# Kernel optimization log

Hardware: AMD Instinct MI355X
Metric: run time of the kernel (lower is better)

## Reference

```python
import jax, jax.numpy as jnp
import numpy as np

B, S, D = 2, 2048, 1024
H, Dh = 16, 64  # qkv_features=1024, head_dim=64
F = 1024        # out_features


def setup_inputs() -> dict:
    key = jax.random.key(0)
    ks = jax.random.split(key, 16)
    s = 0.02
    return {
        'inputs_q': jax.random.normal(ks[0], (B, S, D), jnp.float32),
        'inputs_kv': jax.random.normal(ks[1], (B, S, D), jnp.float32),
        'pos_embed': jax.random.normal(ks[2], (S, D), jnp.float32),
        'Wq': jax.random.normal(ks[3], (D, H, Dh), jnp.float32) * s,
        'bq': jnp.zeros((H, Dh), jnp.float32),
        'Wk': jax.random.normal(ks[4], (D, H, Dh), jnp.float32) * s,
        'bk': jnp.zeros((H, Dh), jnp.float32),
        'Wv': jax.random.normal(ks[5], (D, H, Dh), jnp.float32) * s,
        'bv': jnp.zeros((H, Dh), jnp.float32),
        'Wpos': jax.random.normal(ks[6], (D, H, Dh), jnp.float32) * s,
        'r_r_bias': jax.random.normal(ks[7], (H, Dh), jnp.float32) * s,
        'r_w_bias': jax.random.normal(ks[8], (H, Dh), jnp.float32) * s,
        'Wout': jax.random.normal(ks[9], (H, Dh, F), jnp.float32) * s,
        'bout': jnp.zeros((F,), jnp.float32),
    }


_roll_vmap = jax.vmap(jnp.roll, in_axes=(-2, 0, None), out_axes=-2)


def reference(inputs_q, inputs_kv, pos_embed, Wq, bq, Wk, bk, Wv, bv,
              Wpos, r_r_bias, r_w_bias, Wout, bout):
    # QKV projections: [B,S,D] x [D,H,Dh] -> [B,S,H,Dh]
    q = jnp.einsum('bsd,dhk->bshk', inputs_q, Wq) + bq
    k = jnp.einsum('bsd,dhk->bshk', inputs_kv, Wk) + bk
    v = jnp.einsum('bsd,dhk->bshk', inputs_kv, Wv) + bv
    # relative position embedding projection: [S,D] -> [S,H,Dh]
    r_pos = jnp.einsum('sd,dhk->shk', pos_embed, Wpos)

    q_len = q.shape[-3]
    depth = q.shape[-1]
    # content score + relative-position score, both [B,H,S,S]
    aw = jnp.einsum('bqhd,bkhd->bhqk', q + r_w_bias, k)
    aw_r = jnp.einsum('bqhd,khd->bhqk', q + r_r_bias, r_pos)
    # Transformer-XL relative shift: per query-row roll along key axis
    shifts = jnp.arange(0, q_len) - (q_len - 1)
    aw_r = _roll_vmap(aw_r, shifts, -1)
    aw = (aw + aw_r) / jnp.sqrt(depth).astype(aw.dtype)
    attn = jax.nn.softmax(aw, axis=-1)
    # weighted sum: [B,S,H,Dh]
    x = jnp.einsum('bhqk,bkhd->bqhd', attn, v)
    # output projection contracting (H,Dh)
    out = jnp.einsum('bqhd,hdf->bqf', x, Wout) + bout
    return out
```

## Files before the change

kernel.cpp:

```cpp
#include <hip/hip_runtime.h>
#include <hip/hip_bf16.h>
#include <hip/hip_fp16.h>


#define B_  2
#define S_  2048
#define D_  1024
#define H_  16
#define DH_ 64
#define HD_ 1024
#define F_  1024
#define N_  4096
#define KC_ 512
#define SP2 516
#define KQSC 0.1803368801111204f

typedef __attribute__((ext_vector_type(8))) short  short8;
typedef __attribute__((ext_vector_type(4))) float  floatx4;
typedef __attribute__((ext_vector_type(4))) unsigned int uintx4;

__device__ __forceinline__ unsigned short f2bf(float x) {
  unsigned u = __float_as_uint(x);
  u += 0x7FFFu + ((u >> 16) & 1u);
  return (unsigned short)(u >> 16);
}
__device__ __forceinline__ unsigned short f2h(float x) {
  __half h = __float2half(x);
  unsigned short u; __builtin_memcpy(&u, &h, 2);
  return u;
}
__device__ __forceinline__ float h2f(unsigned short u) {
  __half h; __builtin_memcpy(&h, &u, 2);
  return __half2float(h);
}

#define CQ_ (N_ * D_ / 4)
#define CAST_BLKS 10240
struct PrepP {
  const float* sq; const float* skv; const float* spos;
  unsigned short* dq; unsigned short* dkv; unsigned short* dpos;
  const float* ts[5]; unsigned short* td[5];
};
__global__ void prep_all(PrepP p) {
  __shared__ float t[32][33];
  int bid = blockIdx.x;
  int tid = threadIdx.x;
  if (bid < CAST_BLKS) {
    int i = bid * 256 + tid;
    const float* s; unsigned short* d; int off;
    if (i < CQ_)            { s = p.sq;   d = p.dq;   off = i; }
    else if (i < 2 * CQ_)   { s = p.skv;  d = p.dkv;  off = i - CQ_; }
    else                    { s = p.spos; d = p.dpos; off = i - 2 * CQ_; }
    float4 v = ((const float4*)s)[off];
    ((ushort4*)d)[off] = make_ushort4(f2bf(v.x), f2bf(v.y), f2bf(v.z), f2bf(v.w));
  } else {
    int b2 = bid - CAST_BLKS;
    int z = b2 >> 10, y = (b2 >> 5) & 31, x = b2 & 31;
    const float* src = p.ts[z];
    unsigned short* dst = p.td[z];
    int c0 = x * 32, r0 = y * 32;
    int tx = tid & 31, ty = tid >> 5;
#pragma unroll
    for (int i = 0; i < 4; i++)
      t[ty + i * 8][tx] = src[(size_t)(r0 + ty + i * 8) * 1024 + c0 + tx];
    __syncthreads();
#pragma unroll
    for (int i = 0; i < 4; i++)
      dst[(size_t)(c0 + ty + i * 8) * 1024 + r0 + tx] = f2bf(t[tx][ty + i * 8]);
  }
}

struct GSeg {
  const unsigned short* A; const unsigned short* Bt;
  const float* bias; const float* b2a; const float* b2b;
  unsigned short* outA; unsigned short* outB; float* outF;
  int mode; int bend;
};
struct GP { GSeg s[4]; };
__launch_bounds__(256, 2)
__global__ void gemm_bt(GP p, int Nn, int K) {
  __shared__ unsigned short As[128 * 64];
  __shared__ unsigned short Bs[128 * 64];
  int bx = blockIdx.x;
  GSeg g = p.s[0]; int base = 0;
  if (bx >= p.s[0].bend) { g = p.s[1]; base = p.s[0].bend; }
  if (bx >= p.s[1].bend) { g = p.s[2]; base = p.s[1].bend; }
  if (bx >= p.s[2].bend) { g = p.s[3]; base = p.s[2].bend; }
  bx -= base;
  int nb = Nn >> 7;
  int bm = bx / nb, bn = bx % nb;
  int tid = threadIdx.x;
  int lane = tid & 63, wv = tid >> 6;
  int wm = wv >> 1, wn = wv & 1;
  int lm = lane & 15, lg = lane >> 4;
  const unsigned short* Ab = g.A + (size_t)(bm * 128) * K;
  const unsigned short* Bb = g.Bt + (size_t)(bn * 128) * K;
  floatx4 acc[4][4];
#pragma unroll
  for (int i = 0; i < 4; i++)
#pragma unroll
    for (int j = 0; j < 4; j++) acc[i][j] = (floatx4){0.f, 0.f, 0.f, 0.f};

  int lr = tid >> 3;
  int lc = (tid & 7) * 8;
  for (int k0 = 0; k0 < K; k0 += 64) {
    __syncthreads();
#pragma unroll
    for (int i = 0; i < 4; i++) {
      int r = i * 32 + lr;
      *(uint4*)&As[r * 64 + lc] = *(const uint4*)&Ab[(size_t)r * K + k0 + lc];
      *(uint4*)&Bs[r * 64 + lc] = *(const uint4*)&Bb[(size_t)r * K + k0 + lc];
    }
    __syncthreads();
#pragma unroll
    for (int kk = 0; kk < 2; kk++) {
      short8 af[4], bf[4];
#pragma unroll
      for (int i = 0; i < 4; i++)
        af[i] = *(const short8*)&As[(wm * 64 + i * 16 + lm) * 64 + kk * 32 + lg * 8];
#pragma unroll
      for (int j = 0; j < 4; j++)
        bf[j] = *(const short8*)&Bs[(wn * 64 + j * 16 + lm) * 64 + kk * 32 + lg * 8];
#pragma unroll
      for (int i = 0; i < 4; i++)
#pragma unroll
        for (int j = 0; j < 4; j++)
          acc[i][j] = __builtin_amdgcn_mfma_f32_16x16x32_bf16(af[i], bf[j], acc[i][j], 0, 0, 0);
    }
  }
#pragma unroll
  for (int j = 0; j < 4; j++) {
    int col = bn * 128 + wn * 64 + j * 16 + lm;
    float bs = g.bias ? g.bias[col] : 0.f;
    float ba = g.b2a ? g.b2a[col] : 0.f;
    float bb = g.b2b ? g.b2b[col] : 0.f;
#pragma unroll
    for (int i = 0; i < 4; i++) {
      int row0 = bm * 128 + wm * 64 + i * 16 + lg * 4;
      if (g.mode == 4) {
        int s = row0 & 2047, bb2 = row0 >> 11;
        size_t vidx = (((size_t)bb2 * H_ + (col >> 6)) * 64 + (col & 63)) * (size_t)S_ + s;
        ushort4 o = make_ushort4(f2bf(acc[i][j][0] + bs), f2bf(acc[i][j][1] + bs),
                                 f2bf(acc[i][j][2] + bs), f2bf(acc[i][j][3] + bs));
        *(ushort4*)&g.outA[vidx] = o;
      } else {
#pragma unroll
        for (int r = 0; r < 4; r++) {
          float v = acc[i][j][r] + bs;
          size_t idx = (size_t)(row0 + r) * Nn + col;
          if (g.mode == 0)      g.outA[idx] = f2bf(v);
          else if (g.mode == 1) { g.outA[idx] = f2bf((v + ba) * KQSC); g.outB[idx] = f2bf((v + bb) * KQSC); }
          else                  g.outF[idx] = v;
        }
      }
    }
  }
}

__launch_bounds__(512, 4)
__global__ void attn_kernel(const unsigned short* __restrict__ qw,
                            const unsigned short* __restrict__ qr,
                            const unsigned short* __restrict__ kb,
                            const unsigned short* __restrict__ rb,
                            const unsigned short* __restrict__ vt,
                            unsigned short* __restrict__ xb) {
  __shared__ __align__(16) unsigned short sS[32 * SP2];
  __shared__ float sSum[8][32];
  __shared__ float sLinv[32];
  int bid = blockIdx.x;
  int l = ((bid & 7) << 8) | (bid >> 3);
  int qt = l & 63;
  int bh = l >> 6;
  int b = bh >> 4, h = bh & 15;
  int q0 = qt * 32;
  int tid = threadIdx.x;
  int lane = tid & 63, wv = tid >> 6;
  int lm = lane & 15, lg = lane >> 4;

  short8 bqw[2][2], bqr[2][2];
  const size_t qbase = (size_t)(b * S_ + q0) * HD_ + h * 64;
#pragma unroll
  for (int t = 0; t < 2; t++) {
    const unsigned short* p1 = qw + qbase + (size_t)(t * 16 + lm) * HD_ + lg * 8;
    const unsigned short* p2 = qr + qbase + (size_t)(t * 16 + lm) * HD_ + lg * 8;
    bqw[t][0] = *(const short8*)(p1);
    bqw[t][1] = *(const short8*)(p1 + 32);
    bqr[t][0] = *(const short8*)(p2);
    bqr[t][1] = *(const short8*)(p2 + 32);
  }

  floatx4 acc[2][4];
#pragma unroll
  for (int m = 0; m < 2; m++)
#pragma unroll
    for (int j = 0; j < 4; j++) acc[m][j] = (floatx4){0.f, 0.f, 0.f, 0.f};
  float s0 = 0.f, s1 = 0.f;

  const unsigned short* vb0 = vt + (size_t)(b * H_ + h) * 64 * S_;

  for (int c = 0; c < 4; c++) {
    unsigned short* S = sS;
    int kc = c * KC_;
    for (int jt = wv; jt < 34; jt += 8) {
      int jrow = (kc - q0 - 32 + jt * 16 + lm) & 2047;
      const unsigned short* rp = rb + (size_t)jrow * HD_ + h * 64 + lg * 8;
      short8 a0 = *(const short8*)(rp);
      short8 a1 = *(const short8*)(rp + 32);
#pragma unroll
      for (int t = 0; t < 2; t++) {
        floatx4 c4 = (floatx4){0.f, 0.f, 0.f, 0.f};
        c4 = __builtin_amdgcn_mfma_f32_16x16x32_bf16(a0, bqr[t][0], c4, 0, 0, 0);
        c4 = __builtin_amdgcn_mfma_f32_16x16x32_bf16(a1, bqr[t][1], c4, 0, 0, 0);
        int q = t * 16 + lm;
        int ub = jt * 16 + lg * 4 + q - 31;
        unsigned short* row = &S[q * SP2];
        if (jt + t >= 2 && jt + t <= 32) {
#pragma unroll
          for (int r = 0; r < 4; r++) row[ub + r] = f2h(c4[r]);
        } else {
#pragma unroll
          for (int r = 0; r < 4; r++) {
            int u = ub + r;
            if ((unsigned)u < (unsigned)KC_) row[u] = f2h(c4[r]);
          }
        }
      }
    }
    __syncthreads();
#pragma unroll 2
    for (int kt = 0; kt < 4; kt++) {
      int u0 = wv * 64 + kt * 16;
      const unsigned short* kp = kb + (size_t)(b * S_ + kc + u0 + lm) * HD_ + h * 64 + lg * 8;
      short8 a0 = *(const short8*)(kp);
      short8 a1 = *(const short8*)(kp + 32);
#pragma unroll
      for (int t = 0; t < 2; t++) {
        floatx4 c4 = (floatx4){0.f, 0.f, 0.f, 0.f};
        c4 = __builtin_amdgcn_mfma_f32_16x16x32_bf16(a0, bqw[t][0], c4, 0, 0, 0);
        c4 = __builtin_amdgcn_mfma_f32_16x16x32_bf16(a1, bqw[t][1], c4, 0, 0, 0);
        int q = t * 16 + lm;
        unsigned short* pp = &S[q * SP2 + u0 + lg * 4];
        ushort4 Rv = *(const ushort4*)pp;
        float p0 = exp2f(c4[0] + h2f(Rv.x));
        float p1 = exp2f(c4[1] + h2f(Rv.y));
        float p2 = exp2f(c4[2] + h2f(Rv.z));
        float p3 = exp2f(c4[3] + h2f(Rv.w));
        float ps = (p0 + p1) + (p2 + p3);
        if (t == 0) s0 += ps; else s1 += ps;
        unsigned w0, w1;
        asm("v_cvt_pk_bf16_f32 %0, %1, %2" : "=v"(w0) : "v"(p0), "v"(p1));
        asm("v_cvt_pk_bf16_f32 %0, %1, %2" : "=v"(w1) : "v"(p2), "v"(p3));
        *(uint2*)pp = make_uint2(w0, w1);
      }
    }
#pragma unroll
    for (int s = 0; s < 2; s++) {
      int u0 = wv * 64 + s * 32;
      int e0 = lm * SP2 + u0 + lg * 8;
      int e1 = (16 + lm) * SP2 + u0 + lg * 8;
      uint2 x0 = *(const uint2*)&S[e0];
      uint2 x1 = *(const uint2*)&S[e0 + 4];
      uint2 y0 = *(const uint2*)&S[e1];
      uint2 y1 = *(const uint2*)&S[e1 + 4];
      uintx4 ua = {x0.x, x0.y, x1.x, x1.y};
      uintx4 ub = {y0.x, y0.y, y1.x, y1.y};
      short8 a0 = __builtin_bit_cast(short8, ua);
      short8 a1 = __builtin_bit_cast(short8, ub);
      const unsigned short* vp = vb0 + kc + u0 + lg * 8;
#pragma unroll
      for (int j = 0; j < 4; j++) {
        short8 bb = *(const short8*)&vp[(size_t)(j * 16 + lm) * S_];
        acc[0][j] = __builtin_amdgcn_mfma_f32_16x16x32_bf16(a0, bb, acc[0][j], 0, 0, 0);
        acc[1][j] = __builtin_amdgcn_mfma_f32_16x16x32_bf16(a1, bb, acc[1][j], 0, 0, 0);
      }
    }
    __syncthreads();
  }
  s0 += __shfl_xor(s0, 16); s0 += __shfl_xor(s0, 32);
  s1 += __shfl_xor(s1, 16); s1 += __shfl_xor(s1, 32);
  if (lane < 16) { sSum[wv][lane] = s0; sSum[wv][16 + lane] = s1; }
  float* po = (float*)sS;
  if (wv < 4) {
#pragma unroll
    for (int m = 0; m < 2; m++)
#pragma unroll
      for (int j = 0; j < 4; j++)
#pragma unroll
        for (int r = 0; r < 4; r++) {
          int q = m * 16 + lg * 4 + r;
          int dh = j * 16 + lm;
          po[wv * 2048 + q * 64 + dh] = acc[m][j][r];
        }
  }
  __syncthreads();
  if (tid < 32) {
    float t = 0.f;
#pragma unroll
    for (int w = 0; w < 8; w++) t += sSum[w][tid];
    sLinv[tid] = 1.f / t;
  }
  if (wv >= 4) {
#pragma unroll
    for (int m = 0; m < 2; m++)
#pragma unroll
      for (int j = 0; j < 4; j++)
#pragma unroll
        for (int r = 0; r < 4; r++) {
          int q = m * 16 + lg * 4 + r;
          int dh = j * 16 + lm;
          po[(wv - 4) * 2048 + q * 64 + dh] += acc[m][j][r];
        }
  }
  __syncthreads();
  {
    int e = tid * 4;
    int q = e >> 6, dh = e & 63;
    float4 v = *(float4*)&po[e];
#pragma unroll
    for (int i = 1; i < 4; i++) {
      float4 u = *(float4*)&po[i * 2048 + e];
      v.x += u.x; v.y += u.y; v.z += u.z; v.w += u.w;
    }
    float li = sLinv[q];
    ushort4 o = make_ushort4(f2bf(v.x * li), f2bf(v.y * li), f2bf(v.z * li), f2bf(v.w * li));
    *(ushort4*)&xb[(size_t)(b * S_ + q0 + q) * HD_ + h * 64 + dh] = o;
  }
}

extern "C" void kernel_launch(void* const* d_in, const int* in_sizes, int n_in,
                              void* d_out, int out_size, void* d_ws, size_t ws_size,
                              hipStream_t stream) {
  const float* inputs_q  = (const float*)d_in[0];
  const float* inputs_kv = (const float*)d_in[1];
  const float* pos_embed = (const float*)d_in[2];
  const float* Wq   = (const float*)d_in[3];
  const float* bq   = (const float*)d_in[4];
  const float* Wk   = (const float*)d_in[5];
  const float* bk   = (const float*)d_in[6];
  const float* Wv   = (const float*)d_in[7];
  const float* bv   = (const float*)d_in[8];
  const float* Wpos = (const float*)d_in[9];
  const float* rrb  = (const float*)d_in[10];
  const float* rwb  = (const float*)d_in[11];
  const float* Wout = (const float*)d_in[12];
  const float* bout = (const float*)d_in[13];
  float* out = (float*)d_out;

  char* ws = (char*)d_ws;
  unsigned short* aq  = (unsigned short*)(ws);
  unsigned short* akv = (unsigned short*)(ws + ( 8u << 20));
  unsigned short* apo = (unsigned short*)(ws + (16u << 20));
  unsigned short* wqt = (unsigned short*)(ws + (20u << 20));
  unsigned short* wkt = (unsigned short*)(ws + (22u << 20));
  unsigned short* wvt = (unsigned short*)(ws + (24u << 20));
  unsigned short* wpt = (unsigned short*)(ws + (26u << 20));
  unsigned short* wot = (unsigned short*)(ws + (28u << 20));
  unsigned short* qwp = (unsigned short*)(ws + (30u << 20));
  unsigned short* qrp = (unsigned short*)(ws + (38u << 20));
  unsigned short* kbp = (unsigned short*)(ws + (46u << 20));
  unsigned short* vtp = (unsigned short*)(ws + (54u << 20));
  unsigned short* rbp = (unsigned short*)(ws + (62u << 20));
  unsigned short* xbp = aq;

  PrepP pp;
  pp.sq = inputs_q; pp.skv = inputs_kv; pp.spos = pos_embed;
  pp.dq = aq; pp.dkv = akv; pp.dpos = apo;
  pp.ts[0] = Wq; pp.ts[1] = Wk; pp.ts[2] = Wv; pp.ts[3] = Wpos; pp.ts[4] = Wout;
  pp.td[0] = wqt; pp.td[1] = wkt; pp.td[2] = wvt; pp.td[3] = wpt; pp.td[4] = wot;
  prep_all<<<CAST_BLKS + 5120, 256, 0, stream>>>(pp);

  GP gp{};
  gp.s[0] = {aq,  wqt, bq,      rwb,     rrb,     qwp,     qrp,     nullptr, 1, 256};
  gp.s[1] = {apo, wpt, nullptr, nullptr, nullptr, rbp,     nullptr, nullptr, 0, 384};
  gp.s[2] = {akv, wkt, bk,      nullptr, nullptr, kbp,     nullptr, nullptr, 0, 640};
  gp.s[3] = {akv, wvt, bv,      nullptr, nullptr, vtp,     nullptr, nullptr, 4, 896};
  gemm_bt<<<896, 256, 0, stream>>>(gp, HD_, D_);

  attn_kernel<<<2048, 512, 0, stream>>>(qwp, qrp, kbp, rbp, vtp, xbp);

  GP go{};
  go.s[0] = {xbp, wot, bout, nullptr, nullptr, nullptr, nullptr, out, 2, 256};
  go.s[1] = {nullptr, nullptr, nullptr, nullptr, nullptr, nullptr, nullptr, nullptr, 0, 1 << 30};
  go.s[2] = go.s[1];
  go.s[3] = go.s[1];
  gemm_bt<<<256, 256, 0, stream>>>(go, F_, HD_);
}
```

Measured before the change: 409.7 us.

## Replace separate q+r_r_bias tensor with per-key bias correction and async LDS loads

Uses the identity (q+r_r)·r = (q+r_w)·r + (r_r−r_w)·r. The positional score now reuses the q+r_w operand and adds a per-(head,key) scalar computed by a small new kernel. This removes the second Q output stream from the projection GEMM and the qr loads in attention. The GEMM tile loads switch to global_load_lds direct-to-LDS copies, and attention launch bounds go from 4 to 6 waves per EU, which may increase register pressure. The shared bf16 q operand adds slight rounding differences.

```diff
diff --git a/kernel.cpp b/kernel.cpp
--- a/kernel.cpp
+++ b/kernel.cpp
@@ -32,6 +32,15 @@
 __device__ __forceinline__ float h2f(unsigned short u) {
   __half h; __builtin_memcpy(&h, &u, 2);
   return __half2float(h);
+}
+__device__ __forceinline__ float bf2f(unsigned short u) {
+  return __uint_as_float(((unsigned)u) << 16);
+}
+
+__device__ __forceinline__ void gld_lds16(const void* g, void* l) {
+  __builtin_amdgcn_global_load_lds(
+      (const __attribute__((address_space(1))) unsigned int*)g,
+      (__attribute__((address_space(3))) unsigned int*)l, 16, 0, 0);
 }
 
 #define CQ_ (N_ * D_ / 4)
@@ -70,10 +79,29 @@
   }
 }
 
+__global__ void drp_kernel(const unsigned short* __restrict__ rbp,
+                           const float* __restrict__ rrb, const float* __restrict__ rwb,
+                           float* __restrict__ drp) {
+  int idx = blockIdx.x * 256 + threadIdx.x;
+  int j = idx >> 4, h = idx & 15;
+  const unsigned short* rp = rbp + (size_t)j * HD_ + h * 64;
+  const float* pa = rrb + h * 64;
+  const float* pb = rwb + h * 64;
+  float s = 0.f;
+#pragma unroll
+  for (int k = 0; k < 64; k += 8) {
+    short8 v = *(const short8*)(rp + k);
+#pragma unroll
+    for (int e = 0; e < 8; e++)
+      s += (pa[k + e] - pb[k + e]) * bf2f((unsigned short)v[e]);
+  }
+  drp[h * 2048 + j] = s * KQSC;
+}
+
 struct GSeg {
   const unsigned short* A; const unsigned short* Bt;
-  const float* bias; const float* b2a; const float* b2b;
-  unsigned short* outA; unsigned short* outB; float* outF;
+  const float* bias; const float* b2a;
+  unsigned short* outA; float* outF;
   int mode; int bend;
 };
 struct GP { GSeg s[4]; };
@@ -108,8 +136,8 @@
 #pragma unroll
     for (int i = 0; i < 4; i++) {
       int r = i * 32 + lr;
-      *(uint4*)&As[r * 64 + lc] = *(const uint4*)&Ab[(size_t)r * K + k0 + lc];
-      *(uint4*)&Bs[r * 64 + lc] = *(const uint4*)&Bb[(size_t)r * K + k0 + lc];
+      gld_lds16(&Ab[(size_t)r * K + k0 + lc], &As[r * 64 + lc]);
+      gld_lds16(&Bb[(size_t)r * K + k0 + lc], &Bs[r * 64 + lc]);
     }
     __syncthreads();
 #pragma unroll
@@ -133,7 +161,6 @@
     int col = bn * 128 + wn * 64 + j * 16 + lm;
     float bs = g.bias ? g.bias[col] : 0.f;
     float ba = g.b2a ? g.b2a[col] : 0.f;
-    float bb = g.b2b ? g.b2b[col] : 0.f;
 #pragma unroll
     for (int i = 0; i < 4; i++) {
       int row0 = bm * 128 + wm * 64 + i * 16 + lg * 4;
@@ -149,7 +176,7 @@
           float v = acc[i][j][r] + bs;
           size_t idx = (size_t)(row0 + r) * Nn + col;
           if (g.mode == 0)      g.outA[idx] = f2bf(v);
-          else if (g.mode == 1) { g.outA[idx] = f2bf((v + ba) * KQSC); g.outB[idx] = f2bf((v + bb) * KQSC); }
+          else if (g.mode == 1) g.outA[idx] = f2bf((v + ba) * KQSC);
           else                  g.outF[idx] = v;
         }
       }
@@ -157,12 +184,12 @@
   }
 }
 
-__launch_bounds__(512, 4)
+__launch_bounds__(512, 6)
 __global__ void attn_kernel(const unsigned short* __restrict__ qw,
-                            const unsigned short* __restrict__ qr,
                             const unsigned short* __restrict__ kb,
                             const unsigned short* __restrict__ rb,
                             const unsigned short* __restrict__ vt,
+                            const float* __restrict__ drp,
                             unsigned short* __restrict__ xb) {
   __shared__ __align__(16) unsigned short sS[32 * SP2];
   __shared__ float sSum[8][32];
@@ -177,16 +204,13 @@
   int lane = tid & 63, wv = tid >> 6;
   int lm = lane & 15, lg = lane >> 4;
 
-  short8 bqw[2][2], bqr[2][2];
+  short8 bqw[2][2];
   const size_t qbase = (size_t)(b * S_ + q0) * HD_ + h * 64;
 #pragma unroll
   for (int t = 0; t < 2; t++) {
     const unsigned short* p1 = qw + qbase + (size_t)(t * 16 + lm) * HD_ + lg * 8;
-    const unsigned short* p2 = qr + qbase + (size_t)(t * 16 + lm) * HD_ + lg * 8;
     bqw[t][0] = *(const short8*)(p1);
     bqw[t][1] = *(const short8*)(p1 + 32);
-    bqr[t][0] = *(const short8*)(p2);
-    bqr[t][1] = *(const short8*)(p2 + 32);
   }
 
   floatx4 acc[2][4];
@@ -197,31 +221,34 @@
   float s0 = 0.f, s1 = 0.f;
 
   const unsigned short* vb0 = vt + (size_t)(b * H_ + h) * 64 * S_;
+  const float* drph = drp + h * 2048;
 
   for (int c = 0; c < 4; c++) {
-    unsigned short* S = sS;
     int kc = c * KC_;
     for (int jt = wv; jt < 34; jt += 8) {
-      int jrow = (kc - q0 - 32 + jt * 16 + lm) & 2047;
+      int jb = kc - q0 - 32 + jt * 16;
+      int jrow = (jb + lm) & 2047;
       const unsigned short* rp = rb + (size_t)jrow * HD_ + h * 64 + lg * 8;
       short8 a0 = *(const short8*)(rp);
       short8 a1 = *(const short8*)(rp + 32);
+      int dj = (jb + lg * 4) & 2047;
+      floatx4 dv = *(const floatx4*)&drph[dj];
 #pragma unroll
       for (int t = 0; t < 2; t++) {
         floatx4 c4 = (floatx4){0.f, 0.f, 0.f, 0.f};
-        c4 = __builtin_amdgcn_mfma_f32_16x16x32_bf16(a0, bqr[t][0], c4, 0, 0, 0);
-        c4 = __builtin_amdgcn_mfma_f32_16x16x32_bf16(a1, bqr[t][1], c4, 0, 0, 0);
+        c4 = __builtin_amdgcn_mfma_f32_16x16x32_bf16(a0, bqw[t][0], c4, 0, 0, 0);
+        c4 = __builtin_amdgcn_mfma_f32_16x16x32_bf16(a1, bqw[t][1], c4, 0, 0, 0);
         int q = t * 16 + lm;
         int ub = jt * 16 + lg * 4 + q - 31;
-        unsigned short* row = &S[q * SP2];
+        unsigned short* row = &sS[q * SP2];
         if (jt + t >= 2 && jt + t <= 32) {
 #pragma unroll
-          for (int r = 0; r < 4; r++) row[ub + r] = f2h(c4[r]);
+          for (int r = 0; r < 4; r++) row[ub + r] = f2h(c4[r] + dv[r]);
         } else {
 #pragma unroll
           for (int r = 0; r < 4; r++) {
             int u = ub + r;
-            if ((unsigned)u < (unsigned)KC_) row[u] = f2h(c4[r]);
+            if ((unsigned)u < (unsigned)KC_) row[u] = f2h(c4[r] + dv[r]);
           }
         }
       }
@@ -239,7 +266,7 @@
         c4 = __builtin_amdgcn_mfma_f32_16x16x32_bf16(a0, bqw[t][0], c4, 0, 0, 0);
         c4 = __builtin_amdgcn_mfma_f32_16x16x32_bf16(a1, bqw[t][1], c4, 0, 0, 0);
         int q = t * 16 + lm;
-        unsigned short* pp = &S[q * SP2 + u0 + lg * 4];
+        unsigned short* pp = &sS[q * SP2 + u0 + lg * 4];
         ushort4 Rv = *(const ushort4*)pp;
         float p0 = exp2f(c4[0] + h2f(Rv.x));
         float p1 = exp2f(c4[1] + h2f(Rv.y));
@@ -258,10 +285,10 @@
       int u0 = wv * 64 + s * 32;
       int e0 = lm * SP2 + u0 + lg * 8;
       int e1 = (16 + lm) * SP2 + u0 + lg * 8;
-      uint2 x0 = *(const uint2*)&S[e0];
-      uint2 x1 = *(const uint2*)&S[e0 + 4];
-      uint2 y0 = *(const uint2*)&S[e1];
-      uint2 y1 = *(const uint2*)&S[e1 + 4];
+      uint2 x0 = *(const uint2*)&sS[e0];
+      uint2 x1 = *(const uint2*)&sS[e0 + 4];
+      uint2 y0 = *(const uint2*)&sS[e1];
+      uint2 y1 = *(const uint2*)&sS[e1 + 4];
       uintx4 ua = {x0.x, x0.y, x1.x, x1.y};
       uintx4 ub = {y0.x, y0.y, y1.x, y1.y};
       short8 a0 = __builtin_bit_cast(short8, ua);
@@ -356,7 +383,7 @@
   unsigned short* wpt = (unsigned short*)(ws + (26u << 20));
   unsigned short* wot = (unsigned short*)(ws + (28u << 20));
   unsigned short* qwp = (unsigned short*)(ws + (30u << 20));
-  unsigned short* qrp = (unsigned short*)(ws + (38u << 20));
+  float*          drp = (float*)(ws + (38u << 20));
   unsigned short* kbp = (unsigned short*)(ws + (46u << 20));
   unsigned short* vtp = (unsigned short*)(ws + (54u << 20));
   unsigned short* rbp = (unsigned short*)(ws + (62u << 20));
@@ -370,17 +397,19 @@
   prep_all<<<CAST_BLKS + 5120, 256, 0, stream>>>(pp);
 
   GP gp{};
-  gp.s[0] = {aq,  wqt, bq,      rwb,     rrb,     qwp,     qrp,     nullptr, 1, 256};
-  gp.s[1] = {apo, wpt, nullptr, nullptr, nullptr, rbp,     nullptr, nullptr, 0, 384};
-  gp.s[2] = {akv, wkt, bk,      nullptr, nullptr, kbp,     nullptr, nullptr, 0, 640};
-  gp.s[3] = {akv, wvt, bv,      nullptr, nullptr, vtp,     nullptr, nullptr, 4, 896};
+  gp.s[0] = {aq,  wqt, bq,      rwb,     qwp,     nullptr, 1, 256};
+  gp.s[1] = {apo, wpt, nullptr, nullptr, rbp,     nullptr, 0, 384};
+  gp.s[2] = {akv, wkt, bk,      nullptr, kbp,     nullptr, 0, 640};
+  gp.s[3] = {akv, wvt, bv,      nullptr, vtp,     nullptr, 4, 896};
   gemm_bt<<<896, 256, 0, stream>>>(gp, HD_, D_);
 
-  attn_kernel<<<2048, 512, 0, stream>>>(qwp, qrp, kbp, rbp, vtp, xbp);
+  drp_kernel<<<128, 256, 0, stream>>>(rbp, rrb, rwb, drp);
+
+  attn_kernel<<<2048, 512, 0, stream>>>(qwp, kbp, rbp, vtp, drp, xbp);
 
   GP go{};
-  go.s[0] = {xbp, wot, bout, nullptr, nullptr, nullptr, nullptr, out, 2, 256};
-  go.s[1] = {nullptr, nullptr, nullptr, nullptr, nullptr, nullptr, nullptr, nullptr, 0, 1 << 30};
+  go.s[0] = {xbp, wot, bout, nullptr, nullptr, out, 2, 256};
+  go.s[1] = {nullptr, nullptr, nullptr, nullptr, nullptr, nullptr, 0, 1 << 30};
   go.s[2] = go.s[1];
   go.s[3] = go.s[1];
   gemm_bt<<<256, 256, 0, stream>>>(go, F_, HD_);
```

Result: slower. 515.5 us (+25.8%).
